# Optimization experiments

Hardware: AMD Instinct MI355X
Metric: run time of the kernel (lower is better)

## Reference

```python
import jax, jax.numpy as jnp
import numpy as np

V, D, F, K, L, R, ID, B = 50000, 64, 100, 3, 256, 10, 32, 128
IDMAX = 50


def _cnn(vec, Wc, bc, Wl, bl):
    # vec: [N, L, D] -> Conv1d over L (channels=D), ReLU, max-pool over L, Linear+tanh
    x = vec.transpose(0, 2, 1)  # [N, D, L]
    pad = (K - 1) // 2
    y = jax.lax.conv_general_dilated(x, Wc, (1,), [(pad, pad)],
                                     dimension_numbers=('NCH', 'OIH', 'NCH'))
    y = jax.nn.relu(y + bc[None, :, None])  # [N, F, L]
    y = y.max(axis=2)  # [N, F]
    return jnp.tanh(y @ Wl.T + bl)  # [N, ID]


def _fm(x, v, w, b):
    lin = x @ w.T + b  # [N, 1]
    i1 = x @ v
    i2 = (x ** 2) @ (v ** 2)
    pair = jnp.sum(i1 ** 2 - i2, axis=1)
    return (lin[:, 0] + 0.5 * pair)[:, None]


def setup_inputs() -> dict:
    key = jax.random.key(0)
    ks = iter(jax.random.split(key, 40))
    nrm = lambda shape, s=0.1: jax.random.normal(next(ks), shape, jnp.float32) * s
    ri = lambda shape, hi: jax.random.randint(next(ks), shape, 0, hi, dtype=jnp.int32)
    return dict(
        user_reviews=ri((B, R, L), V), item_reviews=ri((B, R, L), V),
        uids=ri((B,), IDMAX), iids=ri((B,), IDMAX),
        user2item=ri((B, R), IDMAX), item2user=ri((B, R), IDMAX),
        rand_reviews=ri((B, L), V),
        user_emb=nrm((V, D)), item_emb=nrm((V, D)),
        cu_Wc=nrm((F, D, K)), cu_bc=jnp.zeros((F,)), cu_Wl=nrm((ID, F)), cu_bl=jnp.zeros((ID,)),
        ci_Wc=nrm((F, D, K)), ci_bc=jnp.zeros((F,)), ci_Wl=nrm((ID, F)), ci_bl=jnp.zeros((ID,)),
        t_W1=nrm((ID, 2 * R * ID)), t_b1=jnp.full((ID,), 0.1),
        t_W2=nrm((ID, ID)), t_b2=jnp.full((ID,), 0.1),
        fs_v=jnp.full((ID, 8), 0.001), fs_w=nrm((1, ID), 0.001), fs_b=jnp.zeros((1,)),
        te_emb=nrm((V, D)),
        tc_Wc=nrm((F, D, K)), tc_bc=jnp.zeros((F,)), tc_Wl=nrm((ID, F)), tc_bl=jnp.zeros((ID,)),
        ft_v=jnp.full((ID, 8), 0.001), ft_w=nrm((1, ID), 0.001), ft_b=jnp.zeros((1,)),
    )


def reference(user_reviews, item_reviews, uids, iids, user2item, item2user, rand_reviews,
              user_emb, item_emb, cu_Wc, cu_bc, cu_Wl, cu_bl, ci_Wc, ci_bc, ci_Wl, ci_bl,
              t_W1, t_b1, t_W2, t_b2, fs_v, fs_w, fs_b,
              te_emb, tc_Wc, tc_bc, tc_Wl, tc_bl, ft_v, ft_w, ft_b):
    Bn = user_reviews.shape[0]
    ur = user_reviews.reshape(Bn * R, L)
    ir = item_reviews.reshape(Bn * R, L)
    # SourceNet
    ul = _cnn(user_emb[ur], cu_Wc, cu_bc, cu_Wl, cu_bl).reshape(Bn, R * ID)
    il = _cnn(item_emb[ir], ci_Wc, ci_bc, ci_Wl, ci_bl).reshape(Bn, R * ID)
    cat = jnp.concatenate([ul, il], axis=1)  # [B, 2*R*ID]
    h = jnp.tanh(cat @ t_W1.T + t_b1)
    src = jnp.tanh(h @ t_W2.T + t_b2)  # dropout in eval mode = identity
    _src_pred = _fm(jax.lax.stop_gradient(src), fs_v, fs_w, fs_b)  # computed, unused in output
    # Vectorized replacement of the per-sample membership/gather loop
    mu = user2item == iids[:, None]  # [B, R]
    mi = item2user == uids[:, None]  # [B, R]
    gu = user_reviews[jnp.arange(Bn), jnp.argmax(mu, axis=1)]  # first match
    gi = item_reviews[jnp.arange(Bn), jnp.argmax(mi, axis=1)]
    reviews = jnp.where(mu.any(1)[:, None], gu,
                        jnp.where(mi.any(1)[:, None], gi, rand_reviews))  # [B, L]
    # TargetNet
    tl = _cnn(te_emb[reviews], tc_Wc, tc_bc, tc_Wl, tc_bl)
    _tgt_pred = _fm(tl, ft_v, ft_w, ft_b)  # computed, unused in output
    return src, tl
```

## Files before the change

kernel.cpp:

```cpp
#include <hip/hip_runtime.h>
#include <hip/hip_bf16.h>


#define C_V 50000
#define C_D 64
#define C_F 100
#define C_K 3
#define C_L 256
#define C_R 10
#define C_ID 32
#define C_B 128

typedef unsigned int u32;
typedef unsigned short u16;
typedef __attribute__((ext_vector_type(8))) short bf16x8;
typedef __attribute__((ext_vector_type(4))) float f32x4;

__device__ __forceinline__ float bf2f(u16 h) { union {u32 u; float f;} v; v.u = ((u32)h) << 16; return v.f; }
__device__ __forceinline__ u16 f2bf(float f) {
    union {float f; u32 u;} v; v.f = f;
    u32 u = v.u;
    return (u16)((u + 0x7fffu + ((u >> 16) & 1u)) >> 16);
}
__device__ __forceinline__ float ldf(const void* p, int idx, int isf) {
    return isf ? ((const float*)p)[idx] : bf2f(((const u16*)p)[idx]);
}
__device__ __forceinline__ void stf(void* p, int idx, float v, int isf) {
    if (isf) ((float*)p)[idx] = v; else ((u16*)p)[idx] = f2bf(v);
}
__device__ __forceinline__ int detect_isf(const u32* __restrict__ ue, int lane) {
    u32 w = ue[lane];
    u32 e = (w >> 7) & 0xFFu;
    int hit = (e >= 0x70u && e <= 0x7Fu);
    unsigned long long m = __ballot(hit);
    return (__popcll(m) >= 32) ? 0 : 1;
}

__global__ __launch_bounds__(256) void prep_bfrags(
    const void* __restrict__ cu_Wc, const void* __restrict__ ci_Wc,
    const void* __restrict__ tc_Wc, const u32* __restrict__ ue,
    u16* __restrict__ wsB)
{
    int tid = threadIdx.x;
    int isf = detect_isf(ue, tid & 63);
    int id = blockIdx.x * 256 + tid;
    if (id >= 3 * 6 * 7 * 64) return;
    int s    = id / 2688;
    int rem  = id % 2688;
    int c    = rem / 448;
    int rem2 = rem % 448;
    int nt   = rem2 / 64;
    int lane = rem2 % 64;
    int f    = nt * 16 + (lane & 15);
    int quad = lane >> 4;
    const void* W = (s == 0) ? cu_Wc : (s == 1) ? ci_Wc : tc_Wc;
    u16 out[8];
    #pragma unroll
    for (int j = 0; j < 8; ++j) {
        int kdim = c * 32 + quad * 8 + j;
        int tap = kdim >> 6, d = kdim & 63;
        float v = (f < C_F) ? ldf(W, (f * C_D + d) * C_K + tap, isf) : 0.f;
        out[j] = f2bf(v);
    }
    *reinterpret_cast<uint4*>(wsB + id * 8) = *reinterpret_cast<const uint4*>(out);
}

__global__ __launch_bounds__(256, 4) void cnn_mfma(
    const int* __restrict__ user_reviews, const int* __restrict__ item_reviews,
    const int* __restrict__ uids, const int* __restrict__ iids,
    const int* __restrict__ user2item, const int* __restrict__ item2user,
    const int* __restrict__ rand_reviews,
    const void* __restrict__ user_emb, const void* __restrict__ item_emb,
    const void* __restrict__ te_emb,
    const void* __restrict__ cu_bc, const void* __restrict__ cu_Wl, const void* __restrict__ cu_bl,
    const void* __restrict__ ci_bc, const void* __restrict__ ci_Wl, const void* __restrict__ ci_bl,
    const void* __restrict__ tc_bc, const void* __restrict__ tc_Wl, const void* __restrict__ tc_bl,
    const u16* __restrict__ wsB,
    float* __restrict__ ws_cat, void* __restrict__ d_out)
{
    __shared__ __align__(16) char smem[37152 + 1600];
    u16*   embS  = (u16*)smem;
    float* poolS = (float*)(smem + 37152);
    float* partS = (float*)smem;

    const int tid = threadIdx.x;
    const int idx = (blockIdx.x & 7) * 336 + (blockIdx.x >> 3);
    const int lane = tid & 63, wave = tid >> 6;
    const int isf = detect_isf((const u32*)user_emb, lane);

    const int* toks;
    const void* emb;
    int set;
    const void *bc, *Wl, *bl;

    if (idx < C_B * C_R) {
        toks = user_reviews + idx * C_L;
        emb = user_emb; set = 0;
        bc = cu_bc; Wl = cu_Wl; bl = cu_bl;
    } else if (idx < 2 * C_B * C_R) {
        int j = idx - C_B * C_R;
        toks = item_reviews + j * C_L;
        emb = item_emb; set = 1;
        bc = ci_bc; Wl = ci_Wl; bl = ci_bl;
    } else {
        int b = idx - 2 * C_B * C_R;
        const int* t_ = rand_reviews + b * C_L;
        int iid = iids[b];
        int uid = uids[b];
        int fu = -1, fi = -1;
        for (int r = C_R - 1; r >= 0; --r) {
            if (user2item[b * C_R + r] == iid) fu = r;
            if (item2user[b * C_R + r] == uid) fi = r;
        }
        if (fu >= 0)      t_ = user_reviews + (b * C_R + fu) * C_L;
        else if (fi >= 0) t_ = item_reviews + (b * C_R + fi) * C_L;
        toks = t_;
        emb = te_emb; set = 2;
        bc = tc_bc; Wl = tc_Wl; bl = tc_bl;
    }

    if (tid < 36)            ((u32*)embS)[tid] = 0u;
    else if (tid < 72)       ((u32*)embS)[257 * 36 + (tid - 36)] = 0u;

    {
        int token = toks[tid];
        u16* dst = embS + (tid + 1) * 72;
        if (isf) {
            const float4* srow = reinterpret_cast<const float4*>(
                (const float*)emb + (size_t)token * C_D);
            #pragma unroll
            for (int j = 0; j < 8; ++j) {
                float4 a = srow[2 * j];
                float4 b = srow[2 * j + 1];
                u16 t[8] = {f2bf(a.x), f2bf(a.y), f2bf(a.z), f2bf(a.w),
                            f2bf(b.x), f2bf(b.y), f2bf(b.z), f2bf(b.w)};
                *reinterpret_cast<uint4*>(dst + j * 8) = *reinterpret_cast<const uint4*>(t);
            }
        } else {
            const uint4* srow = reinterpret_cast<const uint4*>(
                (const u16*)emb + (size_t)token * C_D);
            #pragma unroll
            for (int j = 0; j < 8; ++j)
                reinterpret_cast<uint4*>(dst)[j] = srow[j];
        }
    }
    __syncthreads();

    const int quad = lane >> 4, mcol = lane & 15;
    const int mbase = wave * 64;
    const u16* BfG = wsB + set * 21504;

    {
        f32x4 acc[4][4];
        #pragma unroll
        for (int mt = 0; mt < 4; ++mt)
            #pragma unroll
            for (int nt = 0; nt < 4; ++nt) acc[mt][nt] = (f32x4){0.f,0.f,0.f,0.f};
        #pragma unroll
        for (int c = 0; c < 6; ++c) {
            const int tap = c >> 1, dh = c & 1;
            bf16x8 bfr[4];
            #pragma unroll
            for (int nt = 0; nt < 4; ++nt)
                bfr[nt] = *reinterpret_cast<const bf16x8*>(BfG + ((c * 7 + nt) * 64 + lane) * 8);
            bf16x8 afr[4];
            #pragma unroll
            for (int mt = 0; mt < 4; ++mt) {
                int row = mbase + mt * 16 + mcol + tap;
                afr[mt] = *reinterpret_cast<const bf16x8*>(embS + row * 72 + dh * 32 + quad * 8);
            }
            #pragma unroll
            for (int mt = 0; mt < 4; ++mt)
                #pragma unroll
                for (int nt = 0; nt < 4; ++nt)
                    acc[mt][nt] = __builtin_amdgcn_mfma_f32_16x16x32_bf16(
                        afr[mt], bfr[nt], acc[mt][nt], 0, 0, 0);
        }
        #pragma unroll
        for (int nt = 0; nt < 4; ++nt) {
            float mv = -1e30f;
            #pragma unroll
            for (int mt = 0; mt < 4; ++mt)
                mv = fmaxf(mv, fmaxf(fmaxf(acc[mt][nt].x, acc[mt][nt].y),
                                     fmaxf(acc[mt][nt].z, acc[mt][nt].w)));
            mv = fmaxf(mv, __shfl_xor(mv, 16));
            mv = fmaxf(mv, __shfl_xor(mv, 32));
            if (quad == 0) poolS[(nt * 16 + mcol) * 4 + wave] = mv;
        }
    }
    {
        f32x4 acc[4][3];
        #pragma unroll
        for (int mt = 0; mt < 4; ++mt)
            #pragma unroll
            for (int nt = 0; nt < 3; ++nt) acc[mt][nt] = (f32x4){0.f,0.f,0.f,0.f};
        #pragma unroll
        for (int c = 0; c < 6; ++c) {
            const int tap = c >> 1, dh = c & 1;
            bf16x8 bfr[3];
            #pragma unroll
            for (int nt = 0; nt < 3; ++nt)
                bfr[nt] = *reinterpret_cast<const bf16x8*>(BfG + ((c * 7 + 4 + nt) * 64 + lane) * 8);
            bf16x8 afr[4];
            #pragma unroll
            for (int mt = 0; mt < 4; ++mt) {
                int row = mbase + mt * 16 + mcol + tap;
                afr[mt] = *reinterpret_cast<const bf16x8*>(embS + row * 72 + dh * 32 + quad * 8);
            }
            #pragma unroll
            for (int mt = 0; mt < 4; ++mt)
                #pragma unroll
                for (int nt = 0; nt < 3; ++nt)
                    acc[mt][nt] = __builtin_amdgcn_mfma_f32_16x16x32_bf16(
                        afr[mt], bfr[nt], acc[mt][nt], 0, 0, 0);
        }
        #pragma unroll
        for (int nt = 0; nt < 3; ++nt) {
            float mv = -1e30f;
            #pragma unroll
            for (int mt = 0; mt < 4; ++mt)
                mv = fmaxf(mv, fmaxf(fmaxf(acc[mt][nt].x, acc[mt][nt].y),
                                     fmaxf(acc[mt][nt].z, acc[mt][nt].w)));
            mv = fmaxf(mv, __shfl_xor(mv, 16));
            mv = fmaxf(mv, __shfl_xor(mv, 32));
            int f = (4 + nt) * 16 + mcol;
            if (quad == 0 && f < C_F) poolS[f * 4 + wave] = mv;
        }
    }
    __syncthreads();

    if (tid < C_F) {
        float m4 = fmaxf(fmaxf(poolS[tid * 4 + 0], poolS[tid * 4 + 1]),
                         fmaxf(poolS[tid * 4 + 2], poolS[tid * 4 + 3]));
        poolS[tid * 4] = fmaxf(m4 + ldf(bc, tid, isf), 0.f);
    }
    __syncthreads();

    {
        int o = tid >> 3, seg = tid & 7;
        int f0 = (seg < 4) ? seg * 13 : 52 + (seg - 4) * 12;
        int cnt = (seg < 4) ? 13 : 12;
        float acc = 0.f;
        for (int q = 0; q < cnt; ++q) {
            int f = f0 + q;
            acc += poolS[f * 4] * ldf(Wl, o * C_F + f, isf);
        }
        partS[o * 8 + seg] = acc;
    }
    __syncthreads();
    if (tid < C_ID) {
        float s = ldf(bl, tid, isf);
        #pragma unroll
        for (int q = 0; q < 8; ++q) s += partS[tid * 8 + q];
        float v = tanhf(s);
        if (idx < C_B * C_R) {
            int b = idx / C_R, r = idx % C_R;
            ws_cat[b * 640 + r * C_ID + tid] = v;
        } else if (idx < 2 * C_B * C_R) {
            int j = idx - C_B * C_R;
            int b = j / C_R, r = j % C_R;
            ws_cat[b * 640 + 320 + r * C_ID + tid] = v;
        } else {
            int b = idx - 2 * C_B * C_R;
            stf(d_out, C_B * C_ID + b * C_ID + tid, v, isf);
        }
    }
}

__global__ __launch_bounds__(256) void head_kernel(
    const float* __restrict__ ws_cat,
    const void* __restrict__ W1, const void* __restrict__ b1,
    const void* __restrict__ W2, const void* __restrict__ b2,
    const u32* __restrict__ ue, void* __restrict__ d_out)
{
    __shared__ float part[C_ID][8];
    __shared__ float h_s[C_ID];
    int b = blockIdx.x;
    int tid = threadIdx.x;
    int isf = detect_isf(ue, tid & 63);
    int o = tid >> 3, seg = tid & 7;
    const float* cat = ws_cat + b * 640;
    float acc = 0.f;
    int j0 = seg * 80;
    for (int j = j0; j < j0 + 80; ++j) acc += cat[j] * ldf(W1, o * 640 + j, isf);
    part[o][seg] = acc;
    __syncthreads();
    if (tid < C_ID) {
        float s = ldf(b1, tid, isf);
        #pragma unroll
        for (int q = 0; q < 8; ++q) s += part[tid][q];
        h_s[tid] = tanhf(s);
    }
    __syncthreads();
    if (tid < C_ID) {
        float s = ldf(b2, tid, isf);
        #pragma unroll
        for (int i = 0; i < C_ID; ++i) s += h_s[i] * ldf(W2, tid * C_ID + i, isf);
        stf(d_out, b * C_ID + tid, tanhf(s), isf);
    }
}

extern "C" void kernel_launch(void* const* d_in, const int* in_sizes, int n_in,
                              void* d_out, int out_size, void* d_ws, size_t ws_size,
                              hipStream_t stream)
{
    const int* user_reviews = (const int*)d_in[0];
    const int* item_reviews = (const int*)d_in[1];
    const int* uids         = (const int*)d_in[2];
    const int* iids         = (const int*)d_in[3];
    const int* user2item    = (const int*)d_in[4];
    const int* item2user    = (const int*)d_in[5];
    const int* rand_reviews = (const int*)d_in[6];
    const void* user_emb = d_in[7];
    const void* item_emb = d_in[8];
    const void* cu_Wc = d_in[9];
    const void* cu_bc = d_in[10];
    const void* cu_Wl = d_in[11];
    const void* cu_bl = d_in[12];
    const void* ci_Wc = d_in[13];
    const void* ci_bc = d_in[14];
    const void* ci_Wl = d_in[15];
    const void* ci_bl = d_in[16];
    const void* t_W1  = d_in[17];
    const void* t_b1  = d_in[18];
    const void* t_W2  = d_in[19];
    const void* t_b2  = d_in[20];
    const void* te_emb = d_in[24];
    const void* tc_Wc  = d_in[25];
    const void* tc_bc  = d_in[26];
    const void* tc_Wl  = d_in[27];
    const void* tc_bl  = d_in[28];

    u16*   ws_B   = (u16*)d_ws;
    float* ws_cat = (float*)((char*)d_ws + 129536);

    prep_bfrags<<<32, 256, 0, stream>>>(cu_Wc, ci_Wc, tc_Wc,
                                        (const u32*)user_emb, ws_B);

    cnn_mfma<<<2 * C_B * C_R + C_B, 256, 0, stream>>>(
        user_reviews, item_reviews, uids, iids, user2item, item2user, rand_reviews,
        user_emb, item_emb, te_emb,
        cu_bc, cu_Wl, cu_bl, ci_bc, ci_Wl, ci_bl, tc_bc, tc_Wl, tc_bl,
        ws_B, ws_cat, d_out);

    head_kernel<<<C_B, 256, 0, stream>>>(ws_cat, t_W1, t_b1, t_W2, t_b2,
                                         (const u32*)user_emb, d_out);
}
```

Baseline: 208.0 us.

## Gather bf16 embedding rows directly into LDS with XOR-swizzled layout

Replaces the padded LDS row layout (stride 72) with an unpadded stride-64 layout that uses XOR chunk swizzling to avoid bank conflicts in MFMA A-fragment reads. For bf16 embeddings it gathers rows with global_load_lds, so the data skips VGPRs and per-thread stores. This targets the cost of the embedding gather stage and reduces LDS footprint, which may allow more occupancy. The risk is that the direct-to-LDS write pattern must line up exactly with the swizzle, and every 16-byte lane load is still a scattered gather.

```diff
diff --git a/kernel.cpp b/kernel.cpp
--- a/kernel.cpp
+++ b/kernel.cpp
@@ -34,6 +34,11 @@
     int hit = (e >= 0x70u && e <= 0x7Fu);
     unsigned long long m = __ballot(hit);
     return (__popcll(m) >= 32) ? 0 : 1;
+}
+__device__ __forceinline__ void gl_lds16(const void* g, void* l) {
+    __builtin_amdgcn_global_load_lds(
+        (const __attribute__((address_space(1))) void*)g,
+        (__attribute__((address_space(3))) void*)l, 16, 0, 0);
 }
 
 __global__ __launch_bounds__(256) void prep_bfrags(
@@ -78,9 +83,9 @@
     const u16* __restrict__ wsB,
     float* __restrict__ ws_cat, void* __restrict__ d_out)
 {
-    __shared__ __align__(16) char smem[37152 + 1600];
+    __shared__ __align__(16) char smem[258 * 128 + 1600];
     u16*   embS  = (u16*)smem;
-    float* poolS = (float*)(smem + 37152);
+    float* poolS = (float*)(smem + 258 * 128);
     float* partS = (float*)smem;
 
     const int tid = threadIdx.x;
@@ -119,29 +124,36 @@
         bc = tc_bc; Wl = tc_Wl; bl = tc_bl;
     }
 
-    if (tid < 36)            ((u32*)embS)[tid] = 0u;
-    else if (tid < 72)       ((u32*)embS)[257 * 36 + (tid - 36)] = 0u;
-
-    {
+    if (tid < 32)            ((u32*)embS)[tid] = 0u;
+    else if (tid < 64)       ((u32*)embS)[257 * 32 + (tid - 32)] = 0u;
+
+    if (!isf) {
+        int tok64 = toks[wave * 64 + lane];
+        const u16* ebp = (const u16*)emb;
+        #pragma unroll
+        for (int i = 0; i < 8; ++i) {
+            int sub = lane >> 3;
+            int token = __shfl(tok64, i * 8 + sub);
+            int row_lds = wave * 64 + i * 8 + sub + 1;
+            int schunk = (lane & 7) ^ (row_lds & 7);
+            const void* g = ebp + (size_t)token * C_D + schunk * 8;
+            u16* ldsbase = embS + (size_t)(wave * 64 + i * 8 + 1) * 64;
+            gl_lds16(g, ldsbase);
+        }
+    } else {
         int token = toks[tid];
-        u16* dst = embS + (tid + 1) * 72;
-        if (isf) {
-            const float4* srow = reinterpret_cast<const float4*>(
-                (const float*)emb + (size_t)token * C_D);
-            #pragma unroll
-            for (int j = 0; j < 8; ++j) {
-                float4 a = srow[2 * j];
-                float4 b = srow[2 * j + 1];
-                u16 t[8] = {f2bf(a.x), f2bf(a.y), f2bf(a.z), f2bf(a.w),
-                            f2bf(b.x), f2bf(b.y), f2bf(b.z), f2bf(b.w)};
-                *reinterpret_cast<uint4*>(dst + j * 8) = *reinterpret_cast<const uint4*>(t);
-            }
-        } else {
-            const uint4* srow = reinterpret_cast<const uint4*>(
-                (const u16*)emb + (size_t)token * C_D);
-            #pragma unroll
-            for (int j = 0; j < 8; ++j)
-                reinterpret_cast<uint4*>(dst)[j] = srow[j];
+        int rw = (tid + 1) & 7;
+        u16* dst = embS + (size_t)(tid + 1) * 64;
+        const float4* srow = reinterpret_cast<const float4*>(
+            (const float*)emb + (size_t)token * C_D);
+        #pragma unroll
+        for (int c = 0; c < 8; ++c) {
+            float4 a = srow[2 * c];
+            float4 b = srow[2 * c + 1];
+            u16 t[8] = {f2bf(a.x), f2bf(a.y), f2bf(a.z), f2bf(a.w),
+                        f2bf(b.x), f2bf(b.y), f2bf(b.z), f2bf(b.w)};
+            *reinterpret_cast<uint4*>(dst + (c ^ rw) * 8) =
+                *reinterpret_cast<const uint4*>(t);
         }
     }
     __syncthreads();
@@ -159,6 +171,7 @@
         #pragma unroll
         for (int c = 0; c < 6; ++c) {
             const int tap = c >> 1, dh = c & 1;
+            const int schunk = (dh * 4 + quad) ^ ((mcol + tap) & 7);
             bf16x8 bfr[4];
             #pragma unroll
             for (int nt = 0; nt < 4; ++nt)
@@ -167,7 +180,7 @@
             #pragma unroll
             for (int mt = 0; mt < 4; ++mt) {
                 int row = mbase + mt * 16 + mcol + tap;
-                afr[mt] = *reinterpret_cast<const bf16x8*>(embS + row * 72 + dh * 32 + quad * 8);
+                afr[mt] = *reinterpret_cast<const bf16x8*>(embS + row * 64 + schunk * 8);
             }
             #pragma unroll
             for (int mt = 0; mt < 4; ++mt)
@@ -197,6 +210,7 @@
         #pragma unroll
         for (int c = 0; c < 6; ++c) {
             const int tap = c >> 1, dh = c & 1;
+            const int schunk = (dh * 4 + quad) ^ ((mcol + tap) & 7);
             bf16x8 bfr[3];
             #pragma unroll
             for (int nt = 0; nt < 3; ++nt)
@@ -205,7 +219,7 @@
             #pragma unroll
             for (int mt = 0; mt < 4; ++mt) {
                 int row = mbase + mt * 16 + mcol + tap;
-                afr[mt] = *reinterpret_cast<const bf16x8*>(embS + row * 72 + dh * 32 + quad * 8);
+                afr[mt] = *reinterpret_cast<const bf16x8*>(embS + row * 64 + schunk * 8);
             }
             #pragma unroll
             for (int mt = 0; mt < 4; ++mt)
```

Result: faster. 202.4 us (-2.7%).

## Load conv A-fragments directly from global embeddings into registers, drop LDS staging

Applied to the files above, without the earlier changes.

Embedding rows are no longer staged in shared memory. Each lane now gathers its MFMA A-fragments for all three taps straight from global memory into a register array, with zeroing at the sequence edges. This removes the LDS write, the barrier and the LDS reads, and shrinks shared memory to the pooling buffers. In exchange each embedding row is loaded three times (once per tap), register pressure rises, and launch bounds drop to 2 blocks per CU.

```diff
diff --git a/kernel.cpp b/kernel.cpp
--- a/kernel.cpp
+++ b/kernel.cpp
@@ -65,7 +65,7 @@
     *reinterpret_cast<uint4*>(wsB + id * 8) = *reinterpret_cast<const uint4*>(out);
 }
 
-__global__ __launch_bounds__(256, 4) void cnn_mfma(
+__global__ __launch_bounds__(256, 2) void cnn_mfma(
     const int* __restrict__ user_reviews, const int* __restrict__ item_reviews,
     const int* __restrict__ uids, const int* __restrict__ iids,
     const int* __restrict__ user2item, const int* __restrict__ item2user,
@@ -78,10 +78,8 @@
     const u16* __restrict__ wsB,
     float* __restrict__ ws_cat, void* __restrict__ d_out)
 {
-    __shared__ __align__(16) char smem[37152 + 1600];
-    u16*   embS  = (u16*)smem;
-    float* poolS = (float*)(smem + 37152);
-    float* partS = (float*)smem;
+    __shared__ float poolS[C_F * 4];
+    __shared__ float partS[C_ID * 8];
 
     const int tid = threadIdx.x;
     const int idx = (blockIdx.x & 7) * 336 + (blockIdx.x >> 3);
@@ -119,35 +117,38 @@
         bc = tc_bc; Wl = tc_Wl; bl = tc_bl;
     }
 
-    if (tid < 36)            ((u32*)embS)[tid] = 0u;
-    else if (tid < 72)       ((u32*)embS)[257 * 36 + (tid - 36)] = 0u;
-
-    {
-        int token = toks[tid];
-        u16* dst = embS + (tid + 1) * 72;
-        if (isf) {
-            const float4* srow = reinterpret_cast<const float4*>(
-                (const float*)emb + (size_t)token * C_D);
-            #pragma unroll
-            for (int j = 0; j < 8; ++j) {
-                float4 a = srow[2 * j];
-                float4 b = srow[2 * j + 1];
-                u16 t[8] = {f2bf(a.x), f2bf(a.y), f2bf(a.z), f2bf(a.w),
-                            f2bf(b.x), f2bf(b.y), f2bf(b.z), f2bf(b.w)};
-                *reinterpret_cast<uint4*>(dst + j * 8) = *reinterpret_cast<const uint4*>(t);
-            }
-        } else {
-            const uint4* srow = reinterpret_cast<const uint4*>(
-                (const u16*)emb + (size_t)token * C_D);
-            #pragma unroll
-            for (int j = 0; j < 8; ++j)
-                reinterpret_cast<uint4*>(dst)[j] = srow[j];
-        }
-    }
-    __syncthreads();
-
     const int quad = lane >> 4, mcol = lane & 15;
     const int mbase = wave * 64;
+
+    bf16x8 afr[6][4];
+    #pragma unroll
+    for (int mt = 0; mt < 4; ++mt) {
+        #pragma unroll
+        for (int tap = 0; tap < 3; ++tap) {
+            int p = mbase + mt * 16 + mcol + tap - 1;
+            int pc = p < 0 ? 0 : (p > 255 ? 255 : p);
+            int tk = toks[pc];
+            bool valid = (p >= 0) && (p <= 255);
+            #pragma unroll
+            for (int dh = 0; dh < 2; ++dh) {
+                int c = tap * 2 + dh;
+                bf16x8 v;
+                if (!isf) {
+                    v = *reinterpret_cast<const bf16x8*>(
+                        (const u16*)emb + (size_t)tk * C_D + dh * 32 + quad * 8);
+                } else {
+                    const float4* fp = reinterpret_cast<const float4*>(
+                        (const float*)emb + (size_t)tk * C_D + dh * 32 + quad * 8);
+                    float4 a = fp[0], b4 = fp[1];
+                    u16 t[8] = {f2bf(a.x), f2bf(a.y), f2bf(a.z), f2bf(a.w),
+                                f2bf(b4.x), f2bf(b4.y), f2bf(b4.z), f2bf(b4.w)};
+                    v = *reinterpret_cast<const bf16x8*>(t);
+                }
+                afr[c][mt] = valid ? v : (bf16x8){0,0,0,0,0,0,0,0};
+            }
+        }
+    }
+
     const u16* BfG = wsB + set * 21504;
 
     {
@@ -158,23 +159,16 @@
             for (int nt = 0; nt < 4; ++nt) acc[mt][nt] = (f32x4){0.f,0.f,0.f,0.f};
         #pragma unroll
         for (int c = 0; c < 6; ++c) {
-            const int tap = c >> 1, dh = c & 1;
             bf16x8 bfr[4];
             #pragma unroll
             for (int nt = 0; nt < 4; ++nt)
                 bfr[nt] = *reinterpret_cast<const bf16x8*>(BfG + ((c * 7 + nt) * 64 + lane) * 8);
-            bf16x8 afr[4];
-            #pragma unroll
-            for (int mt = 0; mt < 4; ++mt) {
-                int row = mbase + mt * 16 + mcol + tap;
-                afr[mt] = *reinterpret_cast<const bf16x8*>(embS + row * 72 + dh * 32 + quad * 8);
-            }
             #pragma unroll
             for (int mt = 0; mt < 4; ++mt)
                 #pragma unroll
                 for (int nt = 0; nt < 4; ++nt)
                     acc[mt][nt] = __builtin_amdgcn_mfma_f32_16x16x32_bf16(
-                        afr[mt], bfr[nt], acc[mt][nt], 0, 0, 0);
+                        afr[c][mt], bfr[nt], acc[mt][nt], 0, 0, 0);
         }
         #pragma unroll
         for (int nt = 0; nt < 4; ++nt) {
@@ -196,23 +190,16 @@
             for (int nt = 0; nt < 3; ++nt) acc[mt][nt] = (f32x4){0.f,0.f,0.f,0.f};
         #pragma unroll
         for (int c = 0; c < 6; ++c) {
-            const int tap = c >> 1, dh = c & 1;
             bf16x8 bfr[3];
             #pragma unroll
             for (int nt = 0; nt < 3; ++nt)
                 bfr[nt] = *reinterpret_cast<const bf16x8*>(BfG + ((c * 7 + 4 + nt) * 64 + lane) * 8);
-            bf16x8 afr[4];
-            #pragma unroll
-            for (int mt = 0; mt < 4; ++mt) {
-                int row = mbase + mt * 16 + mcol + tap;
-                afr[mt] = *reinterpret_cast<const bf16x8*>(embS + row * 72 + dh * 32 + quad * 8);
-            }
             #pragma unroll
             for (int mt = 0; mt < 4; ++mt)
                 #pragma unroll
                 for (int nt = 0; nt < 3; ++nt)
                     acc[mt][nt] = __builtin_amdgcn_mfma_f32_16x16x32_bf16(
-                        afr[mt], bfr[nt], acc[mt][nt], 0, 0, 0);
+                        afr[c][mt], bfr[nt], acc[mt][nt], 0, 0, 0);
         }
         #pragma unroll
         for (int nt = 0; nt < 3; ++nt) {
```

New measurement: 272.3 us. 1.31x slower.
